# Performance work log

Measured on AMD Instinct MI355X. Metric: run time of the kernel, lower is better.

## Reference

```python
import jax, jax.numpy as jnp
import numpy as np

EPS = 1e-5
L = 8      # n_layers
H = 1024   # n_hidden
F_IN = 26  # input features
B = 65536  # batch


def layer_norm(x, gamma, beta):
    m = jnp.mean(x, axis=-1, keepdims=True)
    v = jnp.mean((x - m) ** 2, axis=-1, keepdims=True)
    return (x - m) * jax.lax.rsqrt(v + EPS) * gamma + beta


def setup_inputs() -> dict:
    key = jax.random.key(0)
    ks = jax.random.split(key, 12)
    s_in = 1.0 / np.sqrt(F_IN)
    s_h = 1.0 / np.sqrt(H)
    return {
        "x": jax.random.normal(ks[0], (B, F_IN), jnp.float32),
        "st_gamma": jnp.ones((F_IN,), jnp.float32),
        "st_beta": jnp.zeros((F_IN,), jnp.float32),
        "st_w": jax.random.uniform(ks[1], (H, F_IN), jnp.float32, -s_in, s_in),
        "st_b": jax.random.uniform(ks[2], (H,), jnp.float32, -s_in, s_in),
        "blk_gamma": jnp.ones((L, H), jnp.float32),
        "blk_beta": jnp.zeros((L, H), jnp.float32),
        "blk_w": jax.random.uniform(ks[3], (L, H, H), jnp.float32, -s_h, s_h),
        "blk_b": jax.random.uniform(ks[4], (L, H), jnp.float32, -s_h, s_h),
        "last_gamma": jnp.ones((H,), jnp.float32),
        "last_beta": jnp.zeros((H,), jnp.float32),
        "last_w": jax.random.uniform(ks[5], (1, H), jnp.float32, -s_h, s_h),
        "last_b": jax.random.uniform(ks[6], (1,), jnp.float32, -s_h, s_h),
    }


def reference(x, st_gamma, st_beta, st_w, st_b,
              blk_gamma, blk_beta, blk_w, blk_b,
              last_gamma, last_beta, last_w, last_b):
    # Stem: LN(26) -> Linear(26->H) -> ReLU (dropout = identity in eval)
    h = jax.nn.relu(layer_norm(x, st_gamma, st_beta) @ st_w.T + st_b)

    # n_layers blocks: LN -> Linear(H->H) -> ReLU, scanned over stacked params
    def body(h, params):
        g, b, w, bb = params
        h = jax.nn.relu(layer_norm(h, g, b) @ w.T + bb)
        return h, None

    h, _ = jax.lax.scan(body, h, (blk_gamma, blk_beta, blk_w, blk_b))

    # Head: LN -> Linear(H->1) -> sigmoid
    h = layer_norm(h, last_gamma, last_beta)
    out = jax.nn.sigmoid(h @ last_w.T + last_b)  # [B, 1]
    return out
```

## Files before the change

kernel.cpp:

```cpp
#include <hip/hip_runtime.h>
#include <hip/hip_bf16.h>
#include <stdint.h>


typedef __attribute__((ext_vector_type(8))) _Float16 f16x8;
typedef __attribute__((ext_vector_type(4))) float f32x4;

#define EPSLN 1e-5f
#define HDIM 1024

__device__ __forceinline__ void gload16(const void* g, void* l) {
  __builtin_amdgcn_global_load_lds(
      (const __attribute__((address_space(1))) unsigned int*)g,
      (__attribute__((address_space(3))) unsigned int*)l, 16, 0, 0);
}

__global__ __launch_bounds__(256) void zero_f32(float* __restrict__ p, int n) {
  int i = blockIdx.x * 256 + threadIdx.x;
  if (i < n) p[i] = 0.f;
}

__global__ __launch_bounds__(256) void fold_blk(
    const float* __restrict__ bg, const float* __restrict__ bb,
    const float* __restrict__ bw, const float* __restrict__ bbias,
    _Float16* __restrict__ Wf, float* __restrict__ bfold, float* __restrict__ Sfold) {
  int lo = blockIdx.x;
  int layer = lo >> 10;
  const float* wrow = bw + (size_t)lo * HDIM;
  const float* g = bg + (size_t)layer * HDIM;
  const float* be = bb + (size_t)layer * HDIM;
  _Float16* wout = Wf + (size_t)lo * HDIM;
  int t = threadIdx.x;
  float s = 0.f, acb = 0.f;
  for (int i = t; i < HDIM; i += 256) {
    float wv = wrow[i];
    _Float16 wp = (_Float16)(wv * g[i]);
    wout[i] = wp;
    s += (float)wp;
    acb += be[i] * wv;
  }
#pragma unroll
  for (int off = 1; off < 64; off <<= 1) { s += __shfl_xor(s, off); acb += __shfl_xor(acb, off); }
  __shared__ float rs[4], rb[4];
  int l = t & 63, w = t >> 6;
  if (l == 0) { rs[w] = s; rb[w] = acb; }
  __syncthreads();
  if (t == 0) {
    Sfold[lo] = rs[0] + rs[1] + rs[2] + rs[3];
    bfold[lo] = bbias[lo] + rb[0] + rb[1] + rb[2] + rb[3];
  }
}

__global__ __launch_bounds__(256) void fold_head(
    const float* __restrict__ lg, const float* __restrict__ lb,
    const float* __restrict__ lw, const float* __restrict__ lbias,
    float* __restrict__ headW, float* __restrict__ headAux) {
  int t = threadIdx.x;
  float s = 0.f, acb = 0.f;
  for (int i = t; i < HDIM; i += 256) {
    float wp = lw[i] * lg[i];
    headW[i] = wp;
    s += wp;
    acb += lb[i] * lw[i];
  }
#pragma unroll
  for (int off = 1; off < 64; off <<= 1) { s += __shfl_xor(s, off); acb += __shfl_xor(acb, off); }
  __shared__ float rs[4], rb[4];
  int l = t & 63, w = t >> 6;
  if (l == 0) { rs[w] = s; rb[w] = acb; }
  __syncthreads();
  if (t == 0) {
    headAux[0] = rs[0] + rs[1] + rs[2] + rs[3];
    headAux[1] = lbias[0] + rb[0] + rb[1] + rb[2] + rb[3];
  }
}

__global__ __launch_bounds__(256) void fold_stem(const float* __restrict__ stw,
                                                 _Float16* __restrict__ Wst) {
  int idx = blockIdx.x * 256 + threadIdx.x;
  int o = idx >> 6, i = idx & 63;
  Wst[idx] = (i < 26) ? (_Float16)stw[o * 26 + i] : (_Float16)0.f;
}

__global__ __launch_bounds__(256) void stem_prep(
    const float* __restrict__ x, const float* __restrict__ stg, const float* __restrict__ stb,
    _Float16* __restrict__ xn, int rowBase) {
  __shared__ float xin[128 * 26];
  __shared__ _Float16 xo[128 * 64];
  int t = threadIdx.x;
  const float* src = x + ((size_t)rowBase + (size_t)blockIdx.x * 128) * 26;
  for (int i = t; i < 128 * 26; i += 256) xin[i] = src[i];
  __syncthreads();
  if (t < 128) {
    float m = 0.f;
#pragma unroll
    for (int i = 0; i < 26; ++i) m += xin[t * 26 + i];
    m *= (1.f / 26.f);
    float v = 0.f;
#pragma unroll
    for (int i = 0; i < 26; ++i) { float d = xin[t * 26 + i] - m; v += d * d; }
    float rstd = rsqrtf(v * (1.f / 26.f) + EPSLN);
    _Float16* orow = xo + t * 64;
#pragma unroll
    for (int i = 0; i < 26; ++i)
      orow[i] = (_Float16)((xin[t * 26 + i] - m) * rstd * stg[i] + stb[i]);
#pragma unroll
    for (int i = 26; i < 64; ++i) orow[i] = (_Float16)0.f;
  }
  __syncthreads();
  const float4* s4 = (const float4*)xo;
  float4* d4 = (float4*)(xn + (size_t)blockIdx.x * 128 * 64);
  for (int i = t; i < 1024; i += 256) d4[i] = s4[i];
}

__global__ __launch_bounds__(256) void stem_gemm(
    const _Float16* __restrict__ xn, const _Float16* __restrict__ Wst,
    const float* __restrict__ stbias, _Float16* __restrict__ hout,
    float* __restrict__ stats_out) {
  __shared__ _Float16 As[128 * 64];
  __shared__ _Float16 Bs[128 * 64];
  const int t = threadIdx.x;
  const int l = t & 63;
  const int w = t >> 6;
  const int wm = w >> 1, wn = w & 1;
  const int brow = blockIdx.x * 128;
  const int bcol = blockIdx.y * 128;

  f32x4 acc[4][4];
#pragma unroll
  for (int i = 0; i < 4; ++i)
#pragma unroll
    for (int j = 0; j < 4; ++j) acc[i][j] = (f32x4){0.f, 0.f, 0.f, 0.f};

  const _Float16* ga = xn + (size_t)(brow + (t >> 3)) * 64 + (t & 7) * 8;
  const _Float16* gb = Wst + (size_t)(bcol + (t >> 3)) * 64 + (t & 7) * 8;
  char* lA = (char*)As + (size_t)w * 1024;
  char* lB = (char*)Bs + (size_t)w * 1024;
#pragma unroll
  for (int q = 0; q < 4; ++q) {
    gload16(ga + (size_t)q * 32 * 64, lA + q * 4096);
    gload16(gb + (size_t)q * 32 * 64, lB + q * 4096);
  }
  __syncthreads();

  const int abyte0 = (wm * 64 + (l & 15)) * 128 + (l >> 4) * 16;
  const int bbyte0 = (wn * 64 + (l & 15)) * 128 + (l >> 4) * 16;
#pragma unroll
  for (int ks = 0; ks < 2; ++ks) {
    f16x8 af[4], bfr[4];
#pragma unroll
    for (int m = 0; m < 4; ++m)
      af[m] = *(const f16x8*)((const char*)As + abyte0 + m * 2048 + ks * 64);
#pragma unroll
    for (int n = 0; n < 4; ++n)
      bfr[n] = *(const f16x8*)((const char*)Bs + bbyte0 + n * 2048 + ks * 64);
#pragma unroll
    for (int m = 0; m < 4; ++m)
#pragma unroll
      for (int n = 0; n < 4; ++n)
        acc[m][n] = __builtin_amdgcn_mfma_f32_16x16x32_f16(af[m], bfr[n], acc[m][n], 0, 0, 0);
  }

  float Bf[4];
#pragma unroll
  for (int n = 0; n < 4; ++n) Bf[n] = stbias[bcol + wn * 64 + n * 16 + (l & 15)];
#pragma unroll
  for (int m = 0; m < 4; ++m) {
#pragma unroll
    for (int rg = 0; rg < 4; ++rg) {
      int lrow = brow + wm * 64 + m * 16 + (l >> 4) * 4 + rg;
      float ps = 0.f, psq = 0.f;
#pragma unroll
      for (int n = 0; n < 4; ++n) {
        int col = bcol + wn * 64 + n * 16 + (l & 15);
        float vv = fmaxf(acc[m][n][rg] + Bf[n], 0.f);
        hout[(size_t)lrow * HDIM + col] = (_Float16)vv;
        ps += vv; psq += vv * vv;
      }
#pragma unroll
      for (int off = 1; off < 16; off <<= 1) {
        ps += __shfl_xor(ps, off);
        psq += __shfl_xor(psq, off);
      }
      if ((l & 15) == 0) {
        atomicAdd(&stats_out[lrow * 2 + 0], ps);
        atomicAdd(&stats_out[lrow * 2 + 1], psq);
      }
    }
  }
}

__global__ __launch_bounds__(512, 2) void layer_gemm(
    const _Float16* __restrict__ hin, const float* __restrict__ stats_in,
    const _Float16* __restrict__ W, const float* __restrict__ bfold,
    const float* __restrict__ Sfold, _Float16* __restrict__ hout,
    float* __restrict__ stats_out) {
  __shared__ __align__(128) char smem[2 * 65536];
  const int t = threadIdx.x;
  const int l = t & 63;
  const int w = t >> 6;
  const int wm = w >> 2, wn = w & 3;
  const int bid = blockIdx.x;
  const int brow = (bid >> 2) * 256;
  const int bcol = (bid & 3) * 256;

  f32x4 acc[8][4];
#pragma unroll
  for (int i = 0; i < 8; ++i)
#pragma unroll
    for (int j = 0; j < 4; ++j) acc[i][j] = (f32x4){0.f, 0.f, 0.f, 0.f};

  const int cswz = (t & 7) ^ ((t >> 3) & 7);
  const _Float16* gA = hin + (size_t)(brow + (t >> 3)) * HDIM + cswz * 8;
  const _Float16* gB = W + (size_t)(bcol + (t >> 3)) * HDIM + cswz * 8;
  const int dstw = w << 10;

  auto stageB = [&](int kt, int par) {
    char* d = smem + par * 65536 + 32768 + dstw;
    const _Float16* s = gB + kt * 64;
#pragma unroll
    for (int h = 0; h < 2; ++h) {
      gload16(s + (size_t)(h * 128) * HDIM, d + h * 16384);
      gload16(s + (size_t)(h * 128 + 64) * HDIM, d + h * 16384 + 8192);
    }
  };
  auto stageA = [&](int kt, int par) {
    char* d = smem + par * 65536 + dstw;
    const _Float16* s = gA + kt * 64;
#pragma unroll
    for (int h = 0; h < 2; ++h) {
      gload16(s + (size_t)(h * 128) * HDIM, d + h * 16384);
      gload16(s + (size_t)(h * 128 + 64) * HDIM, d + h * 16384 + 8192);
    }
  };

  const int cx0 = (((l >> 4)) ^ (l & 7)) << 4;
  const int cx1 = ((4 | (l >> 4)) ^ (l & 7)) << 4;
  const int arow = wm * 16384 + (l & 15) * 128;
  const int brow_b = 32768 + wn * 8192 + (l & 15) * 128;

  stageB(0, 0);
  stageA(0, 0);
  asm volatile("s_waitcnt vmcnt(0)" ::: "memory");
  __builtin_amdgcn_s_barrier();

  f16x8 bf[4][2];
  for (int kt = 0; kt < 16; ++kt) {
    const int par = kt & 1;
    const char* bc = smem + par * 65536;
    const bool pf = (kt < 15);
#pragma unroll
    for (int q = 0; q < 4; ++q) {
      f16x8 af[2][2];
      if (q == 0) {
#pragma unroll
        for (int n = 0; n < 4; ++n) {
          bf[n][0] = *(const f16x8*)(bc + brow_b + n * 2048 + cx0);
          bf[n][1] = *(const f16x8*)(bc + brow_b + n * 2048 + cx1);
        }
      }
#pragma unroll
      for (int mm = 0; mm < 2; ++mm) {
        af[mm][0] = *(const f16x8*)(bc + arow + (2 * q + mm) * 2048 + cx0);
        af[mm][1] = *(const f16x8*)(bc + arow + (2 * q + mm) * 2048 + cx1);
      }
      if (q == 0 && pf) stageB(kt + 1, par ^ 1);
      if (q == 1 && pf) stageA(kt + 1, par ^ 1);
      __builtin_amdgcn_s_barrier();
      asm volatile("s_waitcnt lgkmcnt(0)" ::: "memory");
      __builtin_amdgcn_sched_barrier(0);
      __builtin_amdgcn_s_setprio(1);
#pragma unroll
      for (int mm = 0; mm < 2; ++mm)
#pragma unroll
        for (int n = 0; n < 4; ++n) {
          acc[2 * q + mm][n] =
              __builtin_amdgcn_mfma_f32_16x16x32_f16(af[mm][0], bf[n][0], acc[2 * q + mm][n], 0, 0, 0);
          acc[2 * q + mm][n] =
              __builtin_amdgcn_mfma_f32_16x16x32_f16(af[mm][1], bf[n][1], acc[2 * q + mm][n], 0, 0, 0);
        }
      __builtin_amdgcn_s_setprio(0);
      if (q == 3 && pf) asm volatile("s_waitcnt vmcnt(0)" ::: "memory");
      __builtin_amdgcn_s_barrier();
    }
  }

  float* sred = (float*)smem;
  sred[t] = 0.f;
  __syncthreads();

  float Sf[4], Bf2[4];
#pragma unroll
  for (int n = 0; n < 4; ++n) {
    int col = bcol + wn * 64 + n * 16 + (l & 15);
    Sf[n] = Sfold[col];
    Bf2[n] = bfold[col];
  }
#pragma unroll
  for (int m = 0; m < 8; ++m) {
#pragma unroll
    for (int rg = 0; rg < 4; ++rg) {
      int rloc = wm * 128 + m * 16 + (l >> 4) * 4 + rg;
      int grow = brow + rloc;
      float sum = stats_in[(size_t)grow * 2 + 0];
      float sumsq = stats_in[(size_t)grow * 2 + 1];
      float mean = sum * (1.f / 1024.f);
      float rstd = rsqrtf(sumsq * (1.f / 1024.f) - mean * mean + EPSLN);
      float ps = 0.f, psq = 0.f;
#pragma unroll
      for (int n = 0; n < 4; ++n) {
        int col = bcol + wn * 64 + n * 16 + (l & 15);
        float vv = rstd * (acc[m][n][rg] - mean * Sf[n]) + Bf2[n];
        vv = fmaxf(vv, 0.f);
        hout[(size_t)grow * HDIM + col] = (_Float16)vv;
        ps += vv; psq += vv * vv;
      }
#pragma unroll
      for (int off2 = 1; off2 < 16; off2 <<= 1) {
        ps += __shfl_xor(ps, off2);
        psq += __shfl_xor(psq, off2);
      }
      if ((l & 15) == 0) {
        atomicAdd(&sred[rloc * 2 + 0], ps);
        atomicAdd(&sred[rloc * 2 + 1], psq);
      }
    }
  }
  __syncthreads();
  atomicAdd(&stats_out[(size_t)(brow + (t >> 1)) * 2 + (t & 1)], sred[t]);
}

__global__ __launch_bounds__(512) void head_kernel(
    const _Float16* __restrict__ h8, const float* __restrict__ stats8,
    const float* __restrict__ headW, const float* __restrict__ headAux,
    float* __restrict__ out, int rowBase) {
  int t = threadIdx.x, l = t & 63, w = t >> 6;
  int lrow = blockIdx.x * 8 + w;
  const f16x8* hp = (const f16x8*)(h8 + (size_t)lrow * HDIM) + l * 2;
  f16x8 v0 = hp[0], v1 = hp[1];
  float acc = 0.f;
#pragma unroll
  for (int j = 0; j < 8; ++j) acc += (float)v0[j] * headW[l * 16 + j];
#pragma unroll
  for (int j = 0; j < 8; ++j) acc += (float)v1[j] * headW[l * 16 + 8 + j];
#pragma unroll
  for (int off = 1; off < 64; off <<= 1) acc += __shfl_xor(acc, off);
  if (l == 0) {
    float sum = stats8[lrow * 2 + 0], sumsq = stats8[lrow * 2 + 1];
    float mean = sum * (1.f / 1024.f);
    float rstd = rsqrtf(sumsq * (1.f / 1024.f) - mean * mean + EPSLN);
    float z = rstd * (acc - mean * headAux[0]) + headAux[1];
    out[rowBase + lrow] = 1.f / (1.f + expf(-z));
  }
}

extern "C" void kernel_launch(void* const* d_in, const int* in_sizes, int n_in,
                              void* d_out, int out_size, void* d_ws, size_t ws_size,
                              hipStream_t stream) {
  const float* x      = (const float*)d_in[0];
  const float* stg    = (const float*)d_in[1];
  const float* stb    = (const float*)d_in[2];
  const float* stw    = (const float*)d_in[3];
  const float* stbias = (const float*)d_in[4];
  const float* bg     = (const float*)d_in[5];
  const float* bb     = (const float*)d_in[6];
  const float* bw     = (const float*)d_in[7];
  const float* bbias  = (const float*)d_in[8];
  const float* lg     = (const float*)d_in[9];
  const float* lb     = (const float*)d_in[10];
  const float* lw     = (const float*)d_in[11];
  const float* lbias  = (const float*)d_in[12];
  float* out = (float*)d_out;
  const int B = 65536;
  const int L = 8;

  char* ws = (char*)d_ws;
  size_t off = 0;
  auto carve = [&](size_t bytes) -> char* {
    char* p = ws + off;
    off = (off + bytes + 255) & ~(size_t)255;
    return p;
  };
  _Float16* Wf   = (_Float16*)carve((size_t)L * HDIM * HDIM * 2);
  float* bfold   = (float*)carve((size_t)L * HDIM * 4);
  float* Sfold   = (float*)carve((size_t)L * HDIM * 4);
  float* headW   = (float*)carve((size_t)HDIM * 4);
  float* headAux = (float*)carve(256);
  _Float16* Wst  = (_Float16*)carve((size_t)HDIM * 64 * 2);
  size_t fixed = off;

  int R = B;
  while (R > 256) {
    size_t need = fixed + 2 * ((size_t)R * HDIM * 2 + 256) + ((size_t)9 * R * 2 * 4 + 256)
                  + ((size_t)R * 64 * 2 + 256);
    if (need <= ws_size) break;
    R >>= 1;
  }
  _Float16* hA = (_Float16*)carve((size_t)R * HDIM * 2);
  _Float16* hB = (_Float16*)carve((size_t)R * HDIM * 2);
  float* stats = (float*)carve((size_t)9 * R * 2 * 4);
  _Float16* xnb = (_Float16*)carve((size_t)R * 64 * 2);

  fold_blk<<<L * HDIM, 256, 0, stream>>>(bg, bb, bw, bbias, Wf, bfold, Sfold);
  fold_head<<<1, 256, 0, stream>>>(lg, lb, lw, lbias, headW, headAux);
  fold_stem<<<HDIM * 64 / 256, 256, 0, stream>>>(stw, Wst);

  const int nstats = 9 * R * 2;
  for (int c = 0; c < B / R; ++c) {
    int rowBase = c * R;
    zero_f32<<<(nstats + 255) / 256, 256, 0, stream>>>(stats, nstats);
    stem_prep<<<R / 128, 256, 0, stream>>>(x, stg, stb, xnb, rowBase);
    {
      dim3 grid(R / 128, 8);
      stem_gemm<<<grid, 256, 0, stream>>>(xnb, Wst, stbias, hA, stats);
    }
    _Float16* cur = hA;
    _Float16* nxt = hB;
    for (int lyr = 0; lyr < L; ++lyr) {
      int nb = (R / 256) * 4;
      layer_gemm<<<nb, 512, 0, stream>>>(
          cur, stats + (size_t)lyr * R * 2, Wf + (size_t)lyr * HDIM * HDIM,
          bfold + lyr * HDIM, Sfold + lyr * HDIM, nxt, stats + (size_t)(lyr + 1) * R * 2);
      _Float16* tmp = cur; cur = nxt; nxt = tmp;
    }
    head_kernel<<<R / 8, 512, 0, stream>>>(cur, stats + (size_t)8 * R * 2, headW, headAux, out, rowBase);
  }
}
```

Baseline: 1.496 ms.

## Software-pipeline LDS fragment reads across MFMA quarters and remap blocks across XCDs

Replaces the per-quarter barrier/waitcnt structure of the GEMM main loop with a single sync per k-tile. A-fragment LDS reads are double-buffered so the next quarter's reads overlap the current quarter's MFMAs, and both global-to-LDS prefetches are issued together at the start of each tile. Block IDs are also remapped so that consecutive tiles land on the same XCD, which should improve L2 reuse. Fewer barriers cuts stall time, but it relies on the compiler's waitcnt placement and adds register pressure from holding two A-fragment sets.

After: 1.351 ms. 9.7% less time.

```diff
diff --git a/kernel.cpp b/kernel.cpp
--- a/kernel.cpp
+++ b/kernel.cpp
@@ -200,7 +200,11 @@
   const int l = t & 63;
   const int w = t >> 6;
   const int wm = w >> 2, wn = w & 3;
-  const int bid = blockIdx.x;
+  int bid = blockIdx.x;
+  {
+    int nb = gridDim.x;
+    if ((nb & 7) == 0) { int cpx = nb >> 3; bid = (bid & 7) * cpx + (bid >> 3); }
+  }
   const int brow = (bid >> 2) * 256;
   const int bcol = (bid & 3) * 256;
 
@@ -239,51 +243,59 @@
   const int arow = wm * 16384 + (l & 15) * 128;
   const int brow_b = 32768 + wn * 8192 + (l & 15) * 128;
 
+#define READ_AF(dst, q)                                                 \
+  do {                                                                  \
+    dst[0][0] = *(const f16x8*)(bc + arow + (2 * (q)) * 2048 + cx0);    \
+    dst[0][1] = *(const f16x8*)(bc + arow + (2 * (q)) * 2048 + cx1);    \
+    dst[1][0] = *(const f16x8*)(bc + arow + (2 * (q) + 1) * 2048 + cx0);\
+    dst[1][1] = *(const f16x8*)(bc + arow + (2 * (q) + 1) * 2048 + cx1);\
+  } while (0)
+
+#define MFMA_Q(src, q)                                                                          \
+  do {                                                                                          \
+    __builtin_amdgcn_s_setprio(1);                                                              \
+    _Pragma("unroll") for (int mm = 0; mm < 2; ++mm) _Pragma("unroll") for (int n = 0; n < 4;   \
+                                                                            ++n) {              \
+      acc[2 * (q) + mm][n] =                                                                    \
+          __builtin_amdgcn_mfma_f32_16x16x32_f16(src[mm][0], bf[n][0], acc[2 * (q) + mm][n], 0, \
+                                                 0, 0);                                         \
+      acc[2 * (q) + mm][n] =                                                                    \
+          __builtin_amdgcn_mfma_f32_16x16x32_f16(src[mm][1], bf[n][1], acc[2 * (q) + mm][n], 0, \
+                                                 0, 0);                                         \
+    }                                                                                           \
+    __builtin_amdgcn_s_setprio(0);                                                              \
+  } while (0)
+
   stageB(0, 0);
   stageA(0, 0);
-  asm volatile("s_waitcnt vmcnt(0)" ::: "memory");
-  __builtin_amdgcn_s_barrier();
-
-  f16x8 bf[4][2];
+  __syncthreads();
+
   for (int kt = 0; kt < 16; ++kt) {
     const int par = kt & 1;
     const char* bc = smem + par * 65536;
-    const bool pf = (kt < 15);
-#pragma unroll
-    for (int q = 0; q < 4; ++q) {
-      f16x8 af[2][2];
-      if (q == 0) {
-#pragma unroll
-        for (int n = 0; n < 4; ++n) {
-          bf[n][0] = *(const f16x8*)(bc + brow_b + n * 2048 + cx0);
-          bf[n][1] = *(const f16x8*)(bc + brow_b + n * 2048 + cx1);
-        }
-      }
-#pragma unroll
-      for (int mm = 0; mm < 2; ++mm) {
-        af[mm][0] = *(const f16x8*)(bc + arow + (2 * q + mm) * 2048 + cx0);
-        af[mm][1] = *(const f16x8*)(bc + arow + (2 * q + mm) * 2048 + cx1);
-      }
-      if (q == 0 && pf) stageB(kt + 1, par ^ 1);
-      if (q == 1 && pf) stageA(kt + 1, par ^ 1);
-      __builtin_amdgcn_s_barrier();
-      asm volatile("s_waitcnt lgkmcnt(0)" ::: "memory");
-      __builtin_amdgcn_sched_barrier(0);
-      __builtin_amdgcn_s_setprio(1);
-#pragma unroll
-      for (int mm = 0; mm < 2; ++mm)
-#pragma unroll
-        for (int n = 0; n < 4; ++n) {
-          acc[2 * q + mm][n] =
-              __builtin_amdgcn_mfma_f32_16x16x32_f16(af[mm][0], bf[n][0], acc[2 * q + mm][n], 0, 0, 0);
-          acc[2 * q + mm][n] =
-              __builtin_amdgcn_mfma_f32_16x16x32_f16(af[mm][1], bf[n][1], acc[2 * q + mm][n], 0, 0, 0);
-        }
-      __builtin_amdgcn_s_setprio(0);
-      if (q == 3 && pf) asm volatile("s_waitcnt vmcnt(0)" ::: "memory");
-      __builtin_amdgcn_s_barrier();
-    }
-  }
+    f16x8 bf[4][2];
+#pragma unroll
+    for (int n = 0; n < 4; ++n) {
+      bf[n][0] = *(const f16x8*)(bc + brow_b + n * 2048 + cx0);
+      bf[n][1] = *(const f16x8*)(bc + brow_b + n * 2048 + cx1);
+    }
+    f16x8 afA[2][2], afB[2][2];
+    READ_AF(afA, 0);
+    if (kt < 15) {
+      stageB(kt + 1, par ^ 1);
+      stageA(kt + 1, par ^ 1);
+    }
+    READ_AF(afB, 1);
+    MFMA_Q(afA, 0);
+    READ_AF(afA, 2);
+    MFMA_Q(afB, 1);
+    READ_AF(afB, 3);
+    MFMA_Q(afA, 2);
+    MFMA_Q(afB, 3);
+    __syncthreads();
+  }
+#undef READ_AF
+#undef MFMA_Q
 
   float* sred = (float*)smem;
   sred[t] = 0.f;
```

## Restructure layer GEMM into 4-stage K=32 pipeline with XCD-aware block remap

Applied to the files above, without the earlier changes.

Replaces the double-buffered K=64 main loop in layer_gemm with a four-slot ring of K=32 tiles. Each tile is prefetched three steps ahead, and a single barrier per tile waits on a partial vmcnt. Block indices are remapped so consecutive tiles share an XCD for L2 reuse. The stem GEMM now reduces row stats in shared memory before issuing one global atomic per row, and stem_prep uses all 256 threads per block. The cost is a deeper pipeline with narrower K steps, more barriers per K, and changed LDS swizzling.

Result: faster. 1.419 ms (-5.1%).

```diff
diff --git a/kernel.cpp b/kernel.cpp
--- a/kernel.cpp
+++ b/kernel.cpp
@@ -85,13 +85,13 @@
 __global__ __launch_bounds__(256) void stem_prep(
     const float* __restrict__ x, const float* __restrict__ stg, const float* __restrict__ stb,
     _Float16* __restrict__ xn, int rowBase) {
-  __shared__ float xin[128 * 26];
-  __shared__ _Float16 xo[128 * 64];
+  __shared__ float xin[256 * 26];
+  __shared__ _Float16 xo[256 * 64];
   int t = threadIdx.x;
-  const float* src = x + ((size_t)rowBase + (size_t)blockIdx.x * 128) * 26;
-  for (int i = t; i < 128 * 26; i += 256) xin[i] = src[i];
-  __syncthreads();
-  if (t < 128) {
+  const float* src = x + ((size_t)rowBase + (size_t)blockIdx.x * 256) * 26;
+  for (int i = t; i < 256 * 26; i += 256) xin[i] = src[i];
+  __syncthreads();
+  {
     float m = 0.f;
 #pragma unroll
     for (int i = 0; i < 26; ++i) m += xin[t * 26 + i];
@@ -109,8 +109,8 @@
   }
   __syncthreads();
   const float4* s4 = (const float4*)xo;
-  float4* d4 = (float4*)(xn + (size_t)blockIdx.x * 128 * 64);
-  for (int i = t; i < 1024; i += 256) d4[i] = s4[i];
+  float4* d4 = (float4*)(xn + (size_t)blockIdx.x * 256 * 64);
+  for (int i = t; i < 2048; i += 256) d4[i] = s4[i];
 }
 
 __global__ __launch_bounds__(256) void stem_gemm(
@@ -161,6 +161,11 @@
         acc[m][n] = __builtin_amdgcn_mfma_f32_16x16x32_f16(af[m], bfr[n], acc[m][n], 0, 0, 0);
   }
 
+  __syncthreads();
+  float* sred = (float*)As;
+  sred[t] = 0.f;
+  __syncthreads();
+
   float Bf[4];
 #pragma unroll
   for (int n = 0; n < 4; ++n) Bf[n] = stbias[bcol + wn * 64 + n * 16 + (l & 15)];
@@ -168,7 +173,8 @@
   for (int m = 0; m < 4; ++m) {
 #pragma unroll
     for (int rg = 0; rg < 4; ++rg) {
-      int lrow = brow + wm * 64 + m * 16 + (l >> 4) * 4 + rg;
+      int rloc = wm * 64 + m * 16 + (l >> 4) * 4 + rg;
+      int lrow = brow + rloc;
       float ps = 0.f, psq = 0.f;
 #pragma unroll
       for (int n = 0; n < 4; ++n) {
@@ -183,11 +189,13 @@
         psq += __shfl_xor(psq, off);
       }
       if ((l & 15) == 0) {
-        atomicAdd(&stats_out[lrow * 2 + 0], ps);
-        atomicAdd(&stats_out[lrow * 2 + 1], psq);
+        atomicAdd(&sred[rloc * 2 + 0], ps);
+        atomicAdd(&sred[rloc * 2 + 1], psq);
       }
     }
   }
+  __syncthreads();
+  atomicAdd(&stats_out[(size_t)(brow + (t >> 1)) * 2 + (t & 1)], sred[t]);
 }
 
 __global__ __launch_bounds__(512, 2) void layer_gemm(
@@ -195,12 +203,16 @@
     const _Float16* __restrict__ W, const float* __restrict__ bfold,
     const float* __restrict__ Sfold, _Float16* __restrict__ hout,
     float* __restrict__ stats_out) {
-  __shared__ __align__(128) char smem[2 * 65536];
+  __shared__ __align__(128) char smem[4 * 32768];
   const int t = threadIdx.x;
   const int l = t & 63;
   const int w = t >> 6;
   const int wm = w >> 2, wn = w & 3;
-  const int bid = blockIdx.x;
+  int bid = blockIdx.x;
+  {
+    int nb = gridDim.x;
+    if ((nb & 7) == 0) { int cpx = nb >> 3; bid = (bid & 7) * cpx + (bid >> 3); }
+  }
   const int brow = (bid >> 2) * 256;
   const int bcol = (bid & 3) * 256;
 
@@ -210,80 +222,67 @@
 #pragma unroll
     for (int j = 0; j < 4; ++j) acc[i][j] = (f32x4){0.f, 0.f, 0.f, 0.f};
 
-  const int cswz = (t & 7) ^ ((t >> 3) & 7);
-  const _Float16* gA = hin + (size_t)(brow + (t >> 3)) * HDIM + cswz * 8;
-  const _Float16* gB = W + (size_t)(bcol + (t >> 3)) * HDIM + cswz * 8;
+  const int cswz = (t & 3) ^ ((t >> 2) & 3);
+  const _Float16* gA = hin + (size_t)(brow + (t >> 2)) * HDIM + cswz * 8;
+  const _Float16* gB = W + (size_t)(bcol + (t >> 2)) * HDIM + cswz * 8;
   const int dstw = w << 10;
 
-  auto stageB = [&](int kt, int par) {
-    char* d = smem + par * 65536 + 32768 + dstw;
-    const _Float16* s = gB + kt * 64;
-#pragma unroll
-    for (int h = 0; h < 2; ++h) {
-      gload16(s + (size_t)(h * 128) * HDIM, d + h * 16384);
-      gload16(s + (size_t)(h * 128 + 64) * HDIM, d + h * 16384 + 8192);
-    }
+  auto stage = [&](int kt) {
+    char* dA = smem + (kt & 3) * 32768 + dstw;
+    const _Float16* sA = gA + kt * 32;
+    const _Float16* sB = gB + kt * 32;
+    gload16(sA, dA);
+    gload16(sA + (size_t)128 * HDIM, dA + 8192);
+    gload16(sB, dA + 16384);
+    gload16(sB + (size_t)128 * HDIM, dA + 24576);
   };
-  auto stageA = [&](int kt, int par) {
-    char* d = smem + par * 65536 + dstw;
-    const _Float16* s = gA + kt * 64;
-#pragma unroll
-    for (int h = 0; h < 2; ++h) {
-      gload16(s + (size_t)(h * 128) * HDIM, d + h * 16384);
-      gload16(s + (size_t)(h * 128 + 64) * HDIM, d + h * 16384 + 8192);
-    }
+
+  const int cxk = (((l >> 4) ^ (l & 3)) << 4);
+  const int arow0 = wm * 8192 + (l & 15) * 64 + cxk;
+  const int brow0 = 16384 + wn * 4096 + (l & 15) * 64 + cxk;
+
+  auto tile = [&](int kt, bool do_stage) {
+    const char* bc = smem + (kt & 3) * 32768;
+    f16x8 bf[4], af[8];
+#pragma unroll
+    for (int n = 0; n < 4; ++n) bf[n] = *(const f16x8*)(bc + brow0 + n * 1024);
+#pragma unroll
+    for (int m = 0; m < 8; ++m) af[m] = *(const f16x8*)(bc + arow0 + m * 1024);
+    if (do_stage) stage(kt + 3);
+    __builtin_amdgcn_s_setprio(1);
+#pragma unroll
+    for (int m = 0; m < 8; ++m)
+#pragma unroll
+      for (int n = 0; n < 4; ++n)
+        acc[m][n] = __builtin_amdgcn_mfma_f32_16x16x32_f16(af[m], bf[n], acc[m][n], 0, 0, 0);
+    __builtin_amdgcn_s_setprio(0);
   };
 
-  const int cx0 = (((l >> 4)) ^ (l & 7)) << 4;
-  const int cx1 = ((4 | (l >> 4)) ^ (l & 7)) << 4;
-  const int arow = wm * 16384 + (l & 15) * 128;
-  const int brow_b = 32768 + wn * 8192 + (l & 15) * 128;
-
-  stageB(0, 0);
-  stageA(0, 0);
-  asm volatile("s_waitcnt vmcnt(0)" ::: "memory");
-  __builtin_amdgcn_s_barrier();
-
-  f16x8 bf[4][2];
-  for (int kt = 0; kt < 16; ++kt) {
-    const int par = kt & 1;
-    const char* bc = smem + par * 65536;
-    const bool pf = (kt < 15);
-#pragma unroll
-    for (int q = 0; q < 4; ++q) {
-      f16x8 af[2][2];
-      if (q == 0) {
-#pragma unroll
-        for (int n = 0; n < 4; ++n) {
-          bf[n][0] = *(const f16x8*)(bc + brow_b + n * 2048 + cx0);
-          bf[n][1] = *(const f16x8*)(bc + brow_b + n * 2048 + cx1);
-        }
-      }
-#pragma unroll
-      for (int mm = 0; mm < 2; ++mm) {
-        af[mm][0] = *(const f16x8*)(bc + arow + (2 * q + mm) * 2048 + cx0);
-        af[mm][1] = *(const f16x8*)(bc + arow + (2 * q + mm) * 2048 + cx1);
-      }
-      if (q == 0 && pf) stageB(kt + 1, par ^ 1);
-      if (q == 1 && pf) stageA(kt + 1, par ^ 1);
-      __builtin_amdgcn_s_barrier();
-      asm volatile("s_waitcnt lgkmcnt(0)" ::: "memory");
-      __builtin_amdgcn_sched_barrier(0);
-      __builtin_amdgcn_s_setprio(1);
-#pragma unroll
-      for (int mm = 0; mm < 2; ++mm)
-#pragma unroll
-        for (int n = 0; n < 4; ++n) {
-          acc[2 * q + mm][n] =
-              __builtin_amdgcn_mfma_f32_16x16x32_f16(af[mm][0], bf[n][0], acc[2 * q + mm][n], 0, 0, 0);
-          acc[2 * q + mm][n] =
-              __builtin_amdgcn_mfma_f32_16x16x32_f16(af[mm][1], bf[n][1], acc[2 * q + mm][n], 0, 0, 0);
-        }
-      __builtin_amdgcn_s_setprio(0);
-      if (q == 3 && pf) asm volatile("s_waitcnt vmcnt(0)" ::: "memory");
-      __builtin_amdgcn_s_barrier();
-    }
-  }
+#define TILE_BARRIER(N)                                      \
+  do {                                                       \
+    __builtin_amdgcn_sched_barrier(0);                       \
+    asm volatile("s_waitcnt vmcnt(" #N ")" ::: "memory");    \
+    __builtin_amdgcn_s_barrier();                            \
+    __builtin_amdgcn_sched_barrier(0);                       \
+  } while (0)
+
+  stage(0);
+  stage(1);
+  stage(2);
+  TILE_BARRIER(8);
+
+#pragma unroll 1
+  for (int kt = 0; kt < 29; ++kt) {
+    tile(kt, true);
+    TILE_BARRIER(8);
+  }
+  tile(29, false);
+  TILE_BARRIER(4);
+  tile(30, false);
+  TILE_BARRIER(0);
+  tile(31, false);
+  __syncthreads();
+#undef TILE_BARRIER
 
   float* sred = (float*)smem;
   sred[t] = 0.f;
@@ -409,7 +408,7 @@
   for (int c = 0; c < B / R; ++c) {
     int rowBase = c * R;
     zero_f32<<<(nstats + 255) / 256, 256, 0, stream>>>(stats, nstats);
-    stem_prep<<<R / 128, 256, 0, stream>>>(x, stg, stb, xnb, rowBase);
+    stem_prep<<<R / 256, 256, 0, stream>>>(x, stg, stb, xnb, rowBase);
     {
       dim3 grid(R / 128, 8);
       stem_gemm<<<grid, 256, 0, stream>>>(xnb, Wst, stbias, hA, stats);
```
